# Kernel optimization log

Hardware: AMD Instinct MI355X
Metric: run time of the kernel (lower is better)

The kernel has to match this reference:

```python
import jax, jax.numpy as jnp
import numpy as np

T = 1.0
N_NEG = 50
NUM_CLASSES = 500  # smoothing denominator K from CrossEntropyLabelSmooth (faithful quirk)
EPS = 0.1

B, C, D = 2048, 65536, 256


def setup_inputs() -> dict:
    key = jax.random.key(0)
    k1, k2, k3 = jax.random.split(key, 3)
    f = jax.random.normal(k1, (B, D), dtype=jnp.float32)
    centers = jax.random.normal(k2, (C, D), dtype=jnp.float32)
    label = jax.random.randint(k3, (B,), 0, C, dtype=jnp.int64)
    return {"f": f, "centers": centers, "label": label}


def reference(f, centers, label):
    b = f.shape[0]
    rows = jnp.arange(b)
    mat = f @ centers.T                              # [B, C] similarity scores
    pos = mat[rows, label][:, None]                  # [B, 1] positive score
    # mask the positive column so top-k picks only negatives
    masked = mat.at[rows, label].set(-jnp.inf)
    neg, _ = jax.lax.top_k(masked, N_NEG)            # [B, N_neg]
    preds = jnp.concatenate([pos, neg], axis=1) / T  # [B, 1 + N_neg]
    log_probs = jax.nn.log_softmax(preds, axis=1)
    # label-smoothed one-hot with target class 0 (the positive)
    onehot = jnp.zeros_like(log_probs).at[:, 0].set(1.0)
    targets = (1.0 - EPS) * onehot + EPS / NUM_CLASSES
    loss = (-targets * log_probs).mean(0).sum()
    return loss
```

## Files before the change

### kernel.cpp

```cpp
#include <hip/hip_runtime.h>
#include <hip/hip_fp16.h>

#define B_ROWS 2048
#define C_COLS 65536
#define D_DIM  256
#define N_NEG  50
#define NTILES (C_COLS / 128)
#define SN 136

typedef __attribute__((ext_vector_type(8))) short short8;
typedef __attribute__((ext_vector_type(4))) float floatx4;
typedef __fp16 f16x2 __attribute__((ext_vector_type(2)));
typedef __fp16 h8v  __attribute__((ext_vector_type(8)));
typedef __fp16 h4v  __attribute__((ext_vector_type(4)));
typedef __fp16 h2v  __attribute__((ext_vector_type(2)));

__device__ __forceinline__ ushort f2bf(float f) {
  unsigned u = __float_as_uint(f);
  unsigned r = (u + 0x7FFFu + ((u >> 16) & 1u)) >> 16;
  return (ushort)r;
}

__global__ void cvt_swz(const float* __restrict__ in, ushort* __restrict__ out, int n8) {
  int i = blockIdx.x * blockDim.x + threadIdx.x;
  if (i >= n8) return;
  int row = i >> 5;
  int ka  = i & 31;
  int ktile = ka >> 3, kb = ka & 7;
  const float4* src = (const float4*)(in + (size_t)i * 8);
  float4 a = src[0], b = src[1];
  ushort4 o0, o1;
  o0.x = f2bf(a.x); o0.y = f2bf(a.y); o0.z = f2bf(a.z); o0.w = f2bf(a.w);
  o1.x = f2bf(b.x); o1.y = f2bf(b.y); o1.z = f2bf(b.z); o1.w = f2bf(b.w);
  ushort* dst = out + (size_t)row * D_DIM + ktile * 64 + ((kb ^ (row & 7)) << 3);
  ((ushort4*)dst)[0] = o0;
  ((ushort4*)dst)[1] = o1;
}

__device__ __forceinline__ void async16(const void* g, void* l) {
  __builtin_amdgcn_global_load_lds((const __attribute__((address_space(1))) void*)g,
                                   (__attribute__((address_space(3))) void*)l,
                                   16, 0, 0);
}

template <bool PREB>
__global__ void gemm_reduce(const ushort* __restrict__ fb,
                            const ushort* __restrict__ cb,
                            const float* __restrict__ cen,
                            const int* __restrict__ label,
                            float* __restrict__ cand) {
  __shared__ __align__(16) char smem[SN * 128 * 2];
  __shared__ int labLDS[128];
  ushort* Cs = (ushort*)smem;
  ushort* Fs = Cs + 8192;
  ushort* scu = (ushort*)smem;

  const int tid = threadIdx.x, wave = tid >> 6, lane = tid & 63;
  const int l = lane & 15, q = lane >> 4;
  const int m0 = blockIdx.x * 128, n0 = blockIdx.y * 128;
  const int bxTile = blockIdx.y;
  if (tid < 128) labLDS[tid] = label[m0 + tid];

  floatx4 acc[4][4] = {};
  const int wn = (wave >> 1) * 64, wm = (wave & 1) * 64;

  for (int kt = 0; kt < D_DIM / 64; ++kt) {
#pragma unroll
    for (int r = 0; r < 4; ++r) {
      int idx = r * 2048 + wave * 512 + lane * 8;
      int row = idx >> 6, kk = idx & 63;
      async16(fb + (size_t)(m0 + row) * D_DIM + kt * 64 + kk, Fs + r * 2048 + wave * 512);
      if (PREB)
        async16(cb + (size_t)(n0 + row) * D_DIM + kt * 64 + kk, Cs + r * 2048 + wave * 512);
    }
    if (!PREB) {
#pragma unroll
      for (int g = 0; g < 4; ++g) {
        int e = (tid + g * 256) * 8;
        int row = e >> 6, kblk = (e >> 3) & 7;
        const float* gp = cen + (size_t)(n0 + row) * D_DIM + kt * 64 + kblk * 8;
        float4 fa = *(const float4*)gp;
        float4 fbv = *(const float4*)(gp + 4);
        uint4 o;
        o.x = (uint)f2bf(fa.x)  | ((uint)f2bf(fa.y)  << 16);
        o.y = (uint)f2bf(fa.z)  | ((uint)f2bf(fa.w)  << 16);
        o.z = (uint)f2bf(fbv.x) | ((uint)f2bf(fbv.y) << 16);
        o.w = (uint)f2bf(fbv.z) | ((uint)f2bf(fbv.w) << 16);
        *(uint4*)(Cs + (row << 6) + ((kblk ^ (row & 7)) << 3)) = o;
      }
    }
    __syncthreads();

#pragma unroll
    for (int ks = 0; ks < 2; ++ks) {
      short8 a[4], b[4];
#pragma unroll
      for (int i = 0; i < 4; ++i) {
        int swz = ((4 * ks + q) ^ (l & 7)) << 3;
        a[i] = *(const short8*)(Cs + ((wn + i * 16 + l) << 6) + swz);
        b[i] = *(const short8*)(Fs + ((wm + i * 16 + l) << 6) + swz);
      }
#pragma unroll
      for (int i = 0; i < 4; ++i)
#pragma unroll
        for (int j = 0; j < 4; ++j)
          acc[i][j] = __builtin_amdgcn_mfma_f32_16x16x32_bf16(a[i], b[j], acc[i][j], 0, 0, 0);
    }
    __syncthreads();
  }

  __half* sc = (__half*)scu;
#pragma unroll
  for (int i = 0; i < 4; ++i)
#pragma unroll
    for (int j = 0; j < 4; ++j) {
      int mloc = wm + j * 16 + l;
      int nloc = wn + i * 16 + q * 4;
      f16x2 h0 = __builtin_amdgcn_cvt_pkrtz(acc[i][j][0], acc[i][j][1]);
      f16x2 h1 = __builtin_amdgcn_cvt_pkrtz(acc[i][j][2], acc[i][j][3]);
      uint2 w;
      w.x = *(const uint*)&h0;
      w.y = *(const uint*)&h1;
      *(uint2*)(sc + mloc * SN + nloc) = w;
    }
  __syncthreads();

  {
    const int r = tid >> 1, hf = tid & 1;
    const ushort* bp = scu + r * SN + hf * 64;
    const int rel = labLDS[r] - (n0 + hf * 64);
    if ((unsigned)rel < 64u) ((ushort*)bp)[rel] = 0xFC00;
    float outv[4];
#pragma unroll
    for (int g = 0; g < 4; ++g) {
      h8v v0 = ((const h8v*)bp)[g * 2];
      h8v v1 = ((const h8v*)bp)[g * 2 + 1];
      h8v m8 = __builtin_elementwise_max(v0, v1);
      h4v m4 = __builtin_elementwise_max(m8.lo, m8.hi);
      h2v m2 = __builtin_elementwise_max(m4.lo, m4.hi);
      outv[g] = fmaxf((float)m2.x, (float)m2.y);
    }
    *(float4*)(cand + ((size_t)(m0 + r) * NTILES + bxTile) * 8 + hf * 4) =
        make_float4(outv[0], outv[1], outv[2], outv[3]);
  }
}

__device__ __forceinline__ float dec_key(int k) {
  if (k < 0x0400) return -INFINITY;
  ushort h = (k >= 0x8000) ? (ushort)(k ^ 0x8000) : (ushort)(~k & 0xFFFF);
  __half_raw hr; hr.x = h;
  return __half2float((__half)hr);
}

__global__ void final_select(const float* __restrict__ cand, const float* __restrict__ f,
                             const float* __restrict__ cen, const int* __restrict__ label,
                             float* __restrict__ rowloss) {
  __shared__ float sred[8];
  __shared__ int   sint[8];
  const int row = blockIdx.x, tid = threadIdx.x;
  const int lane = tid & 63, wid = tid >> 6;
  const int lab = label[row];

  float v[16];
  const float4* p = (const float4*)(cand + (size_t)row * (NTILES * 8));
#pragma unroll
  for (int g = 0; g < 4; ++g) {
    float4 u = p[tid + g * 256];
    v[g * 4 + 0] = u.x; v[g * 4 + 1] = u.y; v[g * 4 + 2] = u.z; v[g * 4 + 3] = u.w;
  }
  float pv = f[(size_t)row * D_DIM + tid] * cen[(size_t)lab * D_DIM + tid];
  float m = -INFINITY;
#pragma unroll
  for (int k = 0; k < 16; ++k) m = fmaxf(m, v[k]);
#pragma unroll
  for (int o = 32; o > 0; o >>= 1) {
    m = fmaxf(m, __shfl_down(m, o));
    pv += __shfl_down(pv, o);
  }
  if (lane == 0) { sred[wid] = m; sred[4 + wid] = pv; }
  __syncthreads();
  m = fmaxf(fmaxf(sred[0], sred[1]), fmaxf(sred[2], sred[3]));
  const float pos = sred[4] + sred[5] + sred[6] + sred[7];

  __half hm = __float2half(m);
  int hb = (int)(*(ushort*)&hm);
  int km = (m >= 0.f) ? (0x8000 | hb) : (~hb & 0xFFFF);
  int lo = km - 2048, hi = km;
  if (lo < 0x0400) lo = 0x0400;
#pragma unroll
  for (int it = 0; it < 12; ++it) {
    int mid = (lo + hi) >> 1;
    float tau = dec_key(mid);
    int c = 0;
#pragma unroll
    for (int k = 0; k < 16; ++k) c += (v[k] > tau) ? 1 : 0;
#pragma unroll
    for (int o = 32; o > 0; o >>= 1) c += __shfl_down(c, o);
    if (lane == 0) sint[(it & 1) * 4 + wid] = c;
    __syncthreads();
    int base = (it & 1) * 4;
    int tot = sint[base] + sint[base + 1] + sint[base + 2] + sint[base + 3];
    if (tot <= 49) hi = mid; else lo = mid + 1;
  }

  const float tau = dec_key(hi);
  float sum = 0.f, se = 0.f; int c = 0;
#pragma unroll
  for (int k = 0; k < 16; ++k) {
    if (v[k] > tau) { ++c; sum += v[k]; se += expf(v[k] - m); }
  }
#pragma unroll
  for (int o = 32; o > 0; o >>= 1) {
    sum += __shfl_down(sum, o);
    se  += __shfl_down(se, o);
    c   += __shfl_down(c, o);
  }
  if (lane == 0) { sred[wid] = sum; sred[4 + wid] = se; sint[wid] = c; }
  __syncthreads();
  if (tid == 0) {
    float S = sred[0] + sred[1] + sred[2] + sred[3];
    float E = sred[4] + sred[5] + sred[6] + sred[7];
    int   C = sint[0] + sint[1] + sint[2] + sint[3];
    float nfill = (float)(N_NEG - C);
    S += nfill * tau;
    E += nfill * expf(tau - m);
    float M = fmaxf(m, pos);
    float seAll = E * expf(m - M) + expf(pos - M);
    float lse = M + logf(seAll);
    rowloss[row] = 0.9102f * lse - 0.9002f * pos - 2.0e-4f * S;
  }
}

__global__ void sum_loss(const float* __restrict__ rowloss, float* __restrict__ out) {
  __shared__ float red[4];
  const int tid = threadIdx.x;
  float s = 0.f;
  for (int i = tid; i < B_ROWS; i += 256) s += rowloss[i];
#pragma unroll
  for (int o = 32; o > 0; o >>= 1) s += __shfl_down(s, o);
  if ((tid & 63) == 0) red[tid >> 6] = s;
  __syncthreads();
  if (tid == 0) out[0] = (red[0] + red[1] + red[2] + red[3]) * (1.0f / B_ROWS);
}

extern "C" void kernel_launch(void* const* d_in, const int* in_sizes, int n_in,
                              void* d_out, int out_size, void* d_ws, size_t ws_size,
                              hipStream_t stream) {
  const float* f   = (const float*)d_in[0];
  const float* cen = (const float*)d_in[1];
  const int*   label = (const int*)d_in[2];
  float* out = (float*)d_out;

  char* ws = (char*)d_ws;
  float*  cand    = (float*)ws;
  ushort* fb      = (ushort*)(ws + 33554432);
  float*  rowloss = (float*)(ws + 34611200);
  ushort* cb      = (ushort*)(ws + 34619392);
  const bool pre = ws_size >= (34619392ull + 33554432ull);

  cvt_swz<<<256, 256, 0, stream>>>(f, fb, (B_ROWS * D_DIM) / 8);

  dim3 grid(B_ROWS / 128, NTILES);
  if (pre) {
    cvt_swz<<<8192, 256, 0, stream>>>(cen, cb, (C_COLS * D_DIM) / 8);
    gemm_reduce<true><<<grid, 256, 0, stream>>>(fb, cb, cen, label, cand);
  } else {
    gemm_reduce<false><<<grid, 256, 0, stream>>>(fb, nullptr, cen, label, cand);
  }

  final_select<<<B_ROWS, 256, 0, stream>>>(cand, f, cen, label, rowloss);
  sum_loss<<<1, 256, 0, stream>>>(rowloss, out);
}
```

Measured before the change: 202.2 us.

## Reduce GEMM tile maxima in registers, store fp16 candidates, remap block order

The bf16 pre-conversion pass over centers is removed, so centers are always converted inside the GEMM. Their global loads are split into a load phase and a convert phase. The epilogue no longer stages the full score tile in LDS; it masks the label column in registers, reduces 16-column group maxima with cross-lane shuffles, and writes fp16 candidates, halving the candidate buffer traffic. Block indices are remapped so that blocks sharing a centers tile are grouped differently for L2 reuse. The trade-off is that centers are now read as fp32 by every row-block instead of as pre-converted bf16, which raises global traffic.

```diff
diff --git a/kernel.cpp b/kernel.cpp
--- a/kernel.cpp
+++ b/kernel.cpp
@@ -6,19 +6,22 @@
 #define D_DIM  256
 #define N_NEG  50
 #define NTILES (C_COLS / 128)
-#define SN 136
 
 typedef __attribute__((ext_vector_type(8))) short short8;
 typedef __attribute__((ext_vector_type(4))) float floatx4;
 typedef __fp16 f16x2 __attribute__((ext_vector_type(2)));
-typedef __fp16 h8v  __attribute__((ext_vector_type(8)));
-typedef __fp16 h4v  __attribute__((ext_vector_type(4)));
-typedef __fp16 h2v  __attribute__((ext_vector_type(2)));
 
 __device__ __forceinline__ ushort f2bf(float f) {
   unsigned u = __float_as_uint(f);
   unsigned r = (u + 0x7FFFu + ((u >> 16) & 1u)) >> 16;
   return (ushort)r;
+}
+
+__device__ __forceinline__ uint hmax2(uint a, uint b) {
+  union { uint u; f16x2 h; } x, y, r;
+  x.u = a; y.u = b;
+  r.h = __builtin_elementwise_max(x.h, y.h);
+  return r.u;
 }
 
 __global__ void cvt_swz(const float* __restrict__ in, ushort* __restrict__ out, int n8) {
@@ -43,22 +46,23 @@
                                    16, 0, 0);
 }
 
-template <bool PREB>
 __global__ void gemm_reduce(const ushort* __restrict__ fb,
-                            const ushort* __restrict__ cb,
                             const float* __restrict__ cen,
                             const int* __restrict__ label,
-                            float* __restrict__ cand) {
-  __shared__ __align__(16) char smem[SN * 128 * 2];
+                            ushort* __restrict__ cand) {
+  __shared__ __align__(16) ushort Cs[128 * 64];
+  __shared__ __align__(16) ushort Fs[128 * 64];
+  __shared__ __align__(16) ushort gm[128][8];
   __shared__ int labLDS[128];
-  ushort* Cs = (ushort*)smem;
-  ushort* Fs = Cs + 8192;
-  ushort* scu = (ushort*)smem;
 
   const int tid = threadIdx.x, wave = tid >> 6, lane = tid & 63;
   const int l = lane & 15, q = lane >> 4;
-  const int m0 = blockIdx.x * 128, n0 = blockIdx.y * 128;
-  const int bxTile = blockIdx.y;
+
+  const int lin = blockIdx.y * 16 + blockIdx.x;
+  const int lg  = (lin & 7) * 1024 + (lin >> 3);
+  const int m0 = (lg & 15) << 7;
+  const int bxTile = lg >> 4;
+  const int n0 = bxTile << 7;
   if (tid < 128) labLDS[tid] = label[m0 + tid];
 
   floatx4 acc[4][4] = {};
@@ -70,24 +74,25 @@
       int idx = r * 2048 + wave * 512 + lane * 8;
       int row = idx >> 6, kk = idx & 63;
       async16(fb + (size_t)(m0 + row) * D_DIM + kt * 64 + kk, Fs + r * 2048 + wave * 512);
-      if (PREB)
-        async16(cb + (size_t)(n0 + row) * D_DIM + kt * 64 + kk, Cs + r * 2048 + wave * 512);
-    }
-    if (!PREB) {
-#pragma unroll
-      for (int g = 0; g < 4; ++g) {
-        int e = (tid + g * 256) * 8;
-        int row = e >> 6, kblk = (e >> 3) & 7;
-        const float* gp = cen + (size_t)(n0 + row) * D_DIM + kt * 64 + kblk * 8;
-        float4 fa = *(const float4*)gp;
-        float4 fbv = *(const float4*)(gp + 4);
-        uint4 o;
-        o.x = (uint)f2bf(fa.x)  | ((uint)f2bf(fa.y)  << 16);
-        o.y = (uint)f2bf(fa.z)  | ((uint)f2bf(fa.w)  << 16);
-        o.z = (uint)f2bf(fbv.x) | ((uint)f2bf(fbv.y) << 16);
-        o.w = (uint)f2bf(fbv.z) | ((uint)f2bf(fbv.w) << 16);
-        *(uint4*)(Cs + (row << 6) + ((kblk ^ (row & 7)) << 3)) = o;
-      }
+    }
+    float4 ra[4], rb[4];
+#pragma unroll
+    for (int g = 0; g < 4; ++g) {
+      int e = (tid + g * 256) * 8;
+      const float* gp = cen + (size_t)(n0 + (e >> 6)) * D_DIM + kt * 64 + (e & 63);
+      ra[g] = *(const float4*)gp;
+      rb[g] = *(const float4*)(gp + 4);
+    }
+#pragma unroll
+    for (int g = 0; g < 4; ++g) {
+      int e = (tid + g * 256) * 8;
+      int row = e >> 6, kblk = (e >> 3) & 7;
+      uint4 o;
+      o.x = (uint)f2bf(ra[g].x) | ((uint)f2bf(ra[g].y) << 16);
+      o.y = (uint)f2bf(ra[g].z) | ((uint)f2bf(ra[g].w) << 16);
+      o.z = (uint)f2bf(rb[g].x) | ((uint)f2bf(rb[g].y) << 16);
+      o.w = (uint)f2bf(rb[g].z) | ((uint)f2bf(rb[g].w) << 16);
+      *(uint4*)(Cs + (row << 6) + ((kblk ^ (row & 7)) << 3)) = o;
     }
     __syncthreads();
 
@@ -109,39 +114,49 @@
     __syncthreads();
   }
 
-  __half* sc = (__half*)scu;
-#pragma unroll
-  for (int i = 0; i < 4; ++i)
+  int lj[4];
+#pragma unroll
+  for (int j = 0; j < 4; ++j) lj[j] = labLDS[wm + j * 16 + l] - n0 - wn;
+  bool hit = false;
+#pragma unroll
+  for (int j = 0; j < 4; ++j) hit = hit || ((unsigned)lj[j] < 64u);
+  if (__any(hit)) {
 #pragma unroll
     for (int j = 0; j < 4; ++j) {
-      int mloc = wm + j * 16 + l;
-      int nloc = wn + i * 16 + q * 4;
-      f16x2 h0 = __builtin_amdgcn_cvt_pkrtz(acc[i][j][0], acc[i][j][1]);
-      f16x2 h1 = __builtin_amdgcn_cvt_pkrtz(acc[i][j][2], acc[i][j][3]);
-      uint2 w;
-      w.x = *(const uint*)&h0;
-      w.y = *(const uint*)&h1;
-      *(uint2*)(sc + mloc * SN + nloc) = w;
-    }
-  __syncthreads();
-
-  {
-    const int r = tid >> 1, hf = tid & 1;
-    const ushort* bp = scu + r * SN + hf * 64;
-    const int rel = labLDS[r] - (n0 + hf * 64);
-    if ((unsigned)rel < 64u) ((ushort*)bp)[rel] = 0xFC00;
-    float outv[4];
-#pragma unroll
-    for (int g = 0; g < 4; ++g) {
-      h8v v0 = ((const h8v*)bp)[g * 2];
-      h8v v1 = ((const h8v*)bp)[g * 2 + 1];
-      h8v m8 = __builtin_elementwise_max(v0, v1);
-      h4v m4 = __builtin_elementwise_max(m8.lo, m8.hi);
-      h2v m2 = __builtin_elementwise_max(m4.lo, m4.hi);
-      outv[g] = fmaxf((float)m2.x, (float)m2.y);
-    }
-    *(float4*)(cand + ((size_t)(m0 + r) * NTILES + bxTile) * 8 + hf * 4) =
-        make_float4(outv[0], outv[1], outv[2], outv[3]);
+      int relq = lj[j] - q * 4;
+#pragma unroll
+      for (int i = 0; i < 4; ++i) {
+        int rel = relq - i * 16;
+#pragma unroll
+        for (int r = 0; r < 4; ++r)
+          if (rel == r) acc[i][j][r] = -INFINITY;
+      }
+    }
+  }
+#pragma unroll
+  for (int j = 0; j < 4; ++j) {
+    float mx[4];
+#pragma unroll
+    for (int i = 0; i < 4; ++i)
+      mx[i] = fmaxf(fmaxf(acc[i][j][0], acc[i][j][1]),
+                    fmaxf(acc[i][j][2], acc[i][j][3]));
+    union { f16x2 h; uint u; } c0, c1;
+    c0.h = __builtin_amdgcn_cvt_pkrtz(mx[0], mx[1]);
+    c1.h = __builtin_amdgcn_cvt_pkrtz(mx[2], mx[3]);
+    uint u01 = c0.u, u23 = c1.u;
+    u01 = hmax2(u01, __shfl_xor(u01, 16));
+    u01 = hmax2(u01, __shfl_xor(u01, 32));
+    u23 = hmax2(u23, __shfl_xor(u23, 16));
+    u23 = hmax2(u23, __shfl_xor(u23, 32));
+    if (q == 0) {
+      uint2 w; w.x = u01; w.y = u23;
+      *(uint2*)&gm[wm + j * 16 + l][wn >> 4] = w;
+    }
+  }
+  __syncthreads();
+  if (tid < 128) {
+    uint4 w = *(const uint4*)&gm[tid][0];
+    *(uint4*)(cand + ((size_t)(m0 + tid) * NTILES + bxTile) * 8) = w;
   }
 }
 
@@ -152,7 +167,7 @@
   return __half2float((__half)hr);
 }
 
-__global__ void final_select(const float* __restrict__ cand, const float* __restrict__ f,
+__global__ void final_select(const ushort* __restrict__ cand, const float* __restrict__ f,
                              const float* __restrict__ cen, const int* __restrict__ label,
                              float* __restrict__ rowloss) {
   __shared__ float sred[8];
@@ -162,11 +177,15 @@
   const int lab = label[row];
 
   float v[16];
-  const float4* p = (const float4*)(cand + (size_t)row * (NTILES * 8));
-#pragma unroll
-  for (int g = 0; g < 4; ++g) {
-    float4 u = p[tid + g * 256];
-    v[g * 4 + 0] = u.x; v[g * 4 + 1] = u.y; v[g * 4 + 2] = u.z; v[g * 4 + 3] = u.w;
+  const uint4* p = (const uint4*)(cand + (size_t)row * (NTILES * 8));
+#pragma unroll
+  for (int g = 0; g < 2; ++g) {
+    uint4 u = p[tid + g * 256];
+    union { uint u; f16x2 h; } c;
+    c.u = u.x; v[g * 8 + 0] = (float)c.h.x; v[g * 8 + 1] = (float)c.h.y;
+    c.u = u.y; v[g * 8 + 2] = (float)c.h.x; v[g * 8 + 3] = (float)c.h.y;
+    c.u = u.z; v[g * 8 + 4] = (float)c.h.x; v[g * 8 + 5] = (float)c.h.y;
+    c.u = u.w; v[g * 8 + 6] = (float)c.h.x; v[g * 8 + 7] = (float)c.h.y;
   }
   float pv = f[(size_t)row * D_DIM + tid] * cen[(size_t)lab * D_DIM + tid];
   float m = -INFINITY;
@@ -252,21 +271,14 @@
   float* out = (float*)d_out;
 
   char* ws = (char*)d_ws;
-  float*  cand    = (float*)ws;
-  ushort* fb      = (ushort*)(ws + 33554432);
-  float*  rowloss = (float*)(ws + 34611200);
-  ushort* cb      = (ushort*)(ws + 34619392);
-  const bool pre = ws_size >= (34619392ull + 33554432ull);
+  ushort* cand    = (ushort*)ws;
+  ushort* fb      = (ushort*)(ws + 16777216);
+  float*  rowloss = (float*)(ws + 17825792);
 
   cvt_swz<<<256, 256, 0, stream>>>(f, fb, (B_ROWS * D_DIM) / 8);
 
   dim3 grid(B_ROWS / 128, NTILES);
-  if (pre) {
-    cvt_swz<<<8192, 256, 0, stream>>>(cen, cb, (C_COLS * D_DIM) / 8);
-    gemm_reduce<true><<<grid, 256, 0, stream>>>(fb, cb, cen, label, cand);
-  } else {
-    gemm_reduce<false><<<grid, 256, 0, stream>>>(fb, nullptr, cen, label, cand);
-  }
+  gemm_reduce<<<grid, 256, 0, stream>>>(fb, cen, label, cand);
 
   final_select<<<B_ROWS, 256, 0, stream>>>(cand, f, cen, label, rowloss);
   sum_loss<<<1, 256, 0, stream>>>(rowloss, out);
```

Measured after the change: 266.8 us. +32.0%, slower.
